# Kernel optimization log

Measured on AMD Instinct MI355X. Metric: run time of the kernel, lower is better.

Reference implementation:

```python
import jax, jax.numpy as jnp
import numpy as np

N, E, B = 20000, 320000, 64
HID, DEPTH, NFREQ = 128, 4, 8
NODE_DIM, EDGE_DIM, SG = 4, 3, 230
TWO_PI = 2.0 * np.pi


def setup_inputs() -> dict:
    key = jax.random.key(0)
    ks = jax.random.split(key, 20)
    inp = {}
    inp["x"] = jax.random.normal(ks[0], (N, NODE_DIM), jnp.float32)
    inp["edge_index"] = jax.random.randint(ks[1], (2, E), 0, N)
    inp["edge_attr"] = jax.random.normal(ks[2], (E, EDGE_DIM), jnp.float32)
    inp["batch"] = jnp.sort(jax.random.randint(ks[3], (N,), 0, B))
    inp["space_group"] = jax.random.randint(ks[4], (B,), 0, SG)
    inp["node_w"] = jax.random.normal(ks[5], (NODE_DIM, HID), jnp.float32) * 0.1
    inp["node_b"] = jnp.zeros((HID,), jnp.float32)
    inp["sg_table"] = jax.random.normal(ks[6], (SG, HID), jnp.float32) * 0.1
    inp["lin_w"] = jax.random.normal(ks[7], (DEPTH, 2 * HID + EDGE_DIM, HID), jnp.float32) * 0.05
    inp["lin_b"] = jnp.zeros((DEPTH, HID), jnp.float32)
    inp["att_w"] = jax.random.normal(ks[8], (DEPTH, 2 * HID + EDGE_DIM), jnp.float32) * 0.05
    inp["att_b"] = jnp.zeros((DEPTH,), jnp.float32)
    inp["fk_w"] = jax.random.normal(ks[9], (DEPTH, NFREQ, HID, HID), jnp.float32) * 0.1
    inp["fk_b"] = jnp.zeros((DEPTH, HID), jnp.float32)
    inp["bn_g"] = jnp.ones((DEPTH, HID), jnp.float32)
    inp["bn_b"] = jnp.zeros((DEPTH, HID), jnp.float32)
    inp["pool_w"] = jax.random.normal(ks[10], (HID,), jnp.float32) * 0.1
    inp["pool_b"] = jnp.zeros((), jnp.float32)
    inp["head_w1"] = jax.random.normal(ks[11], (4, 2 * HID, HID), jnp.float32) * 0.05
    inp["head_b1"] = jnp.zeros((4, HID), jnp.float32)
    for i, (nm, od) in enumerate([("e", 1), ("s", 3), ("c", 7), ("m", 3)]):
        inp[nm + "_w2"] = jax.random.normal(ks[12 + i], (HID, od), jnp.float32) * 0.05
        inp[nm + "_b2"] = jnp.zeros((od,), jnp.float32)
    return inp


def reference(x, edge_index, edge_attr, batch, space_group, node_w, node_b, sg_table,
              lin_w, lin_b, att_w, att_b, fk_w, fk_b, bn_g, bn_b, pool_w, pool_b,
              head_w1, head_b1, e_w2, e_b2, s_w2, s_b2, c_w2, c_b2, m_w2, m_b2):
    src, dst = edge_index[0], edge_index[1]  # x_j = x[src], x_i = x[dst]
    h = x @ node_w + node_b                  # [N, HID]
    sg = sg_table[space_group]               # [B, HID]
    freqs = jnp.arange(1, NFREQ + 1, dtype=h.dtype)
    for l in range(DEPTH):
        # edge conv: gather-concat-linear-sigmoid attention-scatter add
        tmp = jnp.concatenate([h[dst], h[src], edge_attr], axis=-1)   # [E, 2H+3]
        alpha = jax.nn.sigmoid(tmp @ att_w[l] + att_b[l])[:, None]    # [E, 1]
        msg = alpha * (tmp @ lin_w[l] + lin_b[l])                     # [E, H]
        h_conv = jax.ops.segment_sum(msg, dst, num_segments=N)
        # Fourier-Kolmogorov branch
        ang = TWO_PI * freqs[None, :, None] * h[:, None, :]           # [N, K, H]
        h_fk = (jnp.einsum('nki,kio->no', jnp.sin(ang), fk_w[l])
                + jnp.einsum('nki,kio->no', jnp.cos(ang), fk_w[l]) + fk_b[l])
        h = h_conv + h_fk
        # BatchNorm1d (batch statistics, training semantics) + ReLU; dropout = identity (eval)
        mu = h.mean(axis=0)
        var = h.var(axis=0)
        h = (h - mu) / jnp.sqrt(var + 1e-5) * bn_g[l] + bn_b[l]
        h = jax.nn.relu(h)
    # attention pool: softmax over ALL nodes (dim=0), as in the original
    a = jax.nn.softmax(h @ pool_w + pool_b, axis=0)[:, None]          # [N, 1]
    pooled = jax.ops.segment_sum(a * h, batch, num_segments=B)        # [B, H]
    comb = jnp.concatenate([pooled, sg], axis=-1)                     # [B, 2H]

    def head(i, w2, b2):
        z = jax.nn.relu(comb @ head_w1[i] + head_b1[i])
        return z @ w2 + b2

    energy = head(0, e_w2, e_b2)          # [B, 1]
    stability = head(1, s_w2, s_b2)       # [B, 3]
    crystal_system = head(2, c_w2, c_b2)  # [B, 7]
    material_type = head(3, m_w2, m_b2)   # [B, 3]
    return energy, stability, crystal_system, material_type
```

## Files before the change

### kernel.cpp

```cpp
#include <hip/hip_runtime.h>
#include <math.h>

#define HID 128
#define DEPTH 4
#define PSPLIT 16
#define SMAXB 40

typedef _Float16 half8 __attribute__((ext_vector_type(8)));
typedef float f4 __attribute__((ext_vector_type(4)));

__global__ void k_wsplit(const float* __restrict__ fkw, _Float16* __restrict__ whi,
                         _Float16* __restrict__ wlo) {
    __shared__ float sh[64][65];
    int bid = blockIdx.x;
    int l = bid >> 5; int r = bid & 31; int kb = r >> 1; int nbk = r & 1;
    const float* W = fkw + (size_t)l * 131072;
    _Float16* Hl = whi + (size_t)l * 131072;
    _Float16* Ll = wlo + (size_t)l * 131072;
    int k0 = kb * 64, n0 = nbk * 64;
    for (int i = threadIdx.x; i < 4096; i += 256) {
        int kk = i >> 6, nn = i & 63;
        sh[kk][nn] = W[(k0 + kk) * HID + n0 + nn];
    }
    __syncthreads();
    for (int i = threadIdx.x; i < 4096; i += 256) {
        int nn = i >> 6, kk = i & 63;
        float w = sh[kk][nn];
        _Float16 hi = (_Float16)w;
        _Float16 lo = (_Float16)((w - (float)hi) * 2048.f);
        Hl[(n0 + nn) * 1024 + k0 + kk] = hi;
        Ll[(n0 + nn) * 1024 + k0 + kk] = lo;
    }
}

__global__ void k_wsplit2(const float* __restrict__ linw, _Float16* __restrict__ lwhi,
                          _Float16* __restrict__ lwlo) {
    __shared__ float sh[64][65];
    int bid = blockIdx.x;
    int l = bid >> 3; int r = bid & 7; int cb = r >> 1; int kb = r & 1;
    const float* W = linw + (size_t)l * 259 * HID;
    int c0 = cb * 64, k0 = kb * 64;
    const float* base = W + (size_t)((c0 >= 128) ? 128 : 0) * HID + (c0 & 127);
    for (int i = threadIdx.x; i < 4096; i += 256) {
        int kk = i >> 6, cc = i & 63;
        sh[kk][cc] = base[(size_t)(k0 + kk) * HID + cc];
    }
    __syncthreads();
    _Float16* Hl = lwhi + (size_t)l * 32768;
    _Float16* Ll = lwlo + (size_t)l * 32768;
    for (int i = threadIdx.x; i < 4096; i += 256) {
        int cc = i >> 6, kk = i & 63;
        float w = sh[kk][cc];
        _Float16 hi = (_Float16)w;
        _Float16 lo = (_Float16)((w - (float)hi) * 2048.f);
        Hl[(size_t)(c0 + cc) * 128 + k0 + kk] = hi;
        Ll[(size_t)(c0 + cc) * 128 + k0 + kk] = lo;
    }
}

__global__ void k_hist(const int* __restrict__ dst, int* __restrict__ deg, int E) {
    int e = blockIdx.x * 256 + threadIdx.x;
    if (e < E) atomicAdd(&deg[dst[e]], 1);
}

__global__ void k_scan_a(const int* __restrict__ deg, int* __restrict__ bsum, int N) {
    __shared__ int sh[256];
    int i = blockIdx.x * 256 + threadIdx.x;
    sh[threadIdx.x] = (i < N) ? deg[i] : 0;
    __syncthreads();
    for (int off = 128; off > 0; off >>= 1) {
        if (threadIdx.x < (unsigned)off) sh[threadIdx.x] += sh[threadIdx.x + off];
        __syncthreads();
    }
    if (threadIdx.x == 0) bsum[blockIdx.x] = sh[0];
}

__global__ void k_scan_b(int* __restrict__ bsum, int nb) {
    __shared__ int sh[256];
    int v = (threadIdx.x < (unsigned)nb) ? bsum[threadIdx.x] : 0;
    sh[threadIdx.x] = v;
    __syncthreads();
    for (int off = 1; off < 256; off <<= 1) {
        int add = (threadIdx.x >= (unsigned)off) ? sh[threadIdx.x - off] : 0;
        __syncthreads();
        sh[threadIdx.x] += add;
        __syncthreads();
    }
    if (threadIdx.x < (unsigned)nb) bsum[threadIdx.x] = sh[threadIdx.x] - v;
}

__global__ void k_scan_c(const int* __restrict__ deg, const int* __restrict__ bsum,
                         int* __restrict__ offs, int* __restrict__ cursor, int N) {
    __shared__ int sh[256];
    int i = blockIdx.x * 256 + threadIdx.x;
    int v = (i < N) ? deg[i] : 0;
    sh[threadIdx.x] = v;
    __syncthreads();
    for (int off = 1; off < 256; off <<= 1) {
        int add = (threadIdx.x >= (unsigned)off) ? sh[threadIdx.x - off] : 0;
        __syncthreads();
        sh[threadIdx.x] += add;
        __syncthreads();
    }
    int ex = bsum[blockIdx.x] + sh[threadIdx.x] - v;
    if (i < N) { offs[i] = ex; cursor[i] = ex; }
    if (i == N - 1) offs[N] = ex + v;
}

__global__ void k_scatter(const int* __restrict__ src, const int* __restrict__ dst,
                          const float* __restrict__ ea, int* cursor,
                          int* __restrict__ srco, float4* __restrict__ ea3o, int E) {
    int e = blockIdx.x * 256 + threadIdx.x;
    if (e < E) {
        int d = dst[e];
        int p = atomicAdd(&cursor[d], 1);
        srco[p] = src[e];
        float4 q;
        q.x = ea[e * 3 + 0]; q.y = ea[e * 3 + 1]; q.z = ea[e * 3 + 2]; q.w = 0.f;
        ea3o[p] = q;
    }
}

__global__ void k_bstart(const int* __restrict__ batch, int* __restrict__ boffs, int N, int B) {
    int n = blockIdx.x * 256 + threadIdx.x;
    if (n >= N) return;
    int b1 = batch[n];
    if (n == 0) for (int b = 0; b <= b1; ++b) boffs[b] = 0;
    int b2 = (n + 1 < N) ? batch[n + 1] : B;
    for (int b = b1 + 1; b <= b2; ++b) boffs[b] = n + 1;
}

#define FK_MT 64
__global__ __launch_bounds__(512, 4) void k_gemms(const float* __restrict__ hsrc,
        const float* __restrict__ x, const float* __restrict__ nw, const float* __restrict__ nbv,
        const double* __restrict__ bnst, const float* __restrict__ bng, const float* __restrict__ bnb,
        int mode,
        const _Float16* __restrict__ whi, const _Float16* __restrict__ wlo,
        float* __restrict__ q0, float* __restrict__ q1,
        float* __restrict__ p2, float* __restrict__ p3,
        const _Float16* __restrict__ lwhi, const _Float16* __restrict__ lwlo,
        const float* __restrict__ linb,
        const float* __restrict__ attw, const float* __restrict__ attb,
        float* __restrict__ A1, float* __restrict__ A2,
        float* __restrict__ a1, float* __restrict__ a2,
        int FKB, int N) {
    __shared__ _Float16 ahi[FK_MT * 256];
    __shared__ _Float16 alo[FK_MT * 256];
    __shared__ float s_sc[128], s_sh[128];
    int tid = threadIdx.x;
    if (mode == 1) {
        if (tid < 128) {
            double invN = 1.0 / (double)N;
            float mu = (float)(bnst[tid] * invN);
            float var = (float)(bnst[128 + tid] * invN) - mu * mu;
            float inv = 1.f / sqrtf(var + 1e-5f);
            float sc = bng[tid] * inv;
            s_sc[tid] = sc;
            s_sh[tid] = bnb[tid] - mu * sc;
        }
        __syncthreads();
    }
    if (blockIdx.x < (unsigned)FKB) {
        int bx = blockIdx.x;
        int nb = (bx >> 2) * FK_MT;
        int ks = bx & 3;
        int kbase = ks * 256;
        int fr0 = kbase >> 7;
        {
            int row = tid >> 3;
            int o8 = tid & 7;
            int gn = nb + row;
            int rc = (gn < N) ? gn : (N - 1);
            float hv[2][8];
            if (mode == 0) {
                float4 xr = *(const float4*)&x[(size_t)rc * 4];
#pragma unroll
                for (int s = 0; s < 2; ++s)
#pragma unroll
                    for (int j = 0; j < 8; ++j) {
                        int c = s * 64 + o8 * 8 + j;
                        hv[s][j] = nbv[c] + xr.x * nw[c] + xr.y * nw[HID + c]
                                  + xr.z * nw[2 * HID + c] + xr.w * nw[3 * HID + c];
                    }
            } else {
                const float* hp = hsrc + (size_t)rc * HID + o8 * 8;
                *(float4*)&hv[0][0] = *(const float4*)hp;
                *(float4*)&hv[0][4] = *(const float4*)(hp + 4);
                *(float4*)&hv[1][0] = *(const float4*)(hp + 64);
                *(float4*)&hv[1][4] = *(const float4*)(hp + 68);
#pragma unroll
                for (int s = 0; s < 2; ++s)
#pragma unroll
                    for (int j = 0; j < 8; ++j) {
                        int c = s * 64 + o8 * 8 + j;
                        hv[s][j] = fmaxf(hv[s][j] * s_sc[c] + s_sh[c], 0.f);
                    }
            }
            int rs = row & 7;
#pragma unroll
            for (int g = 0; g < 2; ++g) {
                float freqf = 6.2831853f * (float)(fr0 + g + 1);
#pragma unroll
                for (int s = 0; s < 2; ++s) {
                    half8 vh, vl;
#pragma unroll
                    for (int j = 0; j < 8; ++j) {
                        float ang = freqf * hv[s][j] + 0.78539816f;
                        float a = 1.41421356f * __sinf(ang);
                        _Float16 hi = (_Float16)a;
                        vh[j] = hi;
                        vl[j] = (_Float16)((a - (float)hi) * 2048.f);
                    }
                    int oct = (g * 16 + s * 8 + o8) ^ rs;
                    *(half8*)&ahi[row * 256 + oct * 8] = vh;
                    *(half8*)&alo[row * 256 + oct * 8] = vl;
                }
            }
        }
        __syncthreads();
        int lane = tid & 63, wv = tid >> 6;
        int quad = lane >> 4, l16 = lane & 15;
        int n0w = wv * 16;
        f4 acc0[4], accL[4];
#pragma unroll
        for (int mi = 0; mi < 4; ++mi) { acc0[mi] = (f4)(0.f); accL[mi] = (f4)(0.f); }
        const _Float16* bhp = whi + (size_t)(n0w + l16) * 1024 + kbase + quad * 8;
        const _Float16* blp = wlo + (size_t)(n0w + l16) * 1024 + kbase + quad * 8;
        int rs16 = (l16 & 7) << 3;
#pragma unroll 2
        for (int step = 0; step < 8; ++step) {
            int ka = (step * 32 + quad * 8) ^ rs16;
            int ko = step * 32;
            half8 bh = *(const half8*)(bhp + ko);
            half8 bl = *(const half8*)(blp + ko);
            half8 ah[4], al[4];
#pragma unroll
            for (int mi = 0; mi < 4; ++mi) {
                ah[mi] = *(const half8*)&ahi[(l16 + mi * 16) * 256 + ka];
                al[mi] = *(const half8*)&alo[(l16 + mi * 16) * 256 + ka];
            }
#pragma unroll
            for (int mi = 0; mi < 4; ++mi) {
                acc0[mi] = __builtin_amdgcn_mfma_f32_16x16x32_f16(ah[mi], bh, acc0[mi], 0, 0, 0);
                accL[mi] = __builtin_amdgcn_mfma_f32_16x16x32_f16(ah[mi], bl, accL[mi], 0, 0, 0);
                accL[mi] = __builtin_amdgcn_mfma_f32_16x16x32_f16(al[mi], bh, accL[mi], 0, 0, 0);
            }
        }
        float* p = (ks == 0) ? q0 : (ks == 1) ? q1 : (ks == 2) ? p2 : p3;
        const float inv = 1.0f / 2048.0f;
#pragma unroll
        for (int mi = 0; mi < 4; ++mi)
#pragma unroll
            for (int r = 0; r < 4; ++r) {
                int gn = nb + mi * 16 + quad * 4 + r;
                if (gn < N)
                    p[gn * HID + n0w + l16] = acc0[mi][r] + accL[mi][r] * inv;
            }
    } else {
        int nb = (blockIdx.x - FKB) * 32;
        {
            int row = tid >> 4;
            int o16 = tid & 15;
            int gn = nb + row;
            int rc = (gn < N) ? gn : (N - 1);
            float hv[8];
            if (mode == 0) {
                float4 xr = *(const float4*)&x[(size_t)rc * 4];
#pragma unroll
                for (int j = 0; j < 8; ++j) {
                    int c = o16 * 8 + j;
                    hv[j] = nbv[c] + xr.x * nw[c] + xr.y * nw[HID + c]
                           + xr.z * nw[2 * HID + c] + xr.w * nw[3 * HID + c];
                }
            } else {
                const float* hp = hsrc + (size_t)rc * HID + o16 * 8;
                *(float4*)&hv[0] = *(const float4*)hp;
                *(float4*)&hv[4] = *(const float4*)(hp + 4);
#pragma unroll
                for (int j = 0; j < 8; ++j) {
                    int c = o16 * 8 + j;
                    hv[j] = fmaxf(hv[j] * s_sc[c] + s_sh[c], 0.f);
                }
            }
            float p1 = 0.f, p2d = 0.f;
#pragma unroll
            for (int j = 0; j < 8; ++j) {
                int k = o16 * 8 + j;
                p1 += hv[j] * attw[k];
                p2d += hv[j] * attw[128 + k];
            }
            for (int off = 8; off > 0; off >>= 1) {
                p1 += __shfl_down(p1, off, 16);
                p2d += __shfl_down(p2d, off, 16);
            }
            if (o16 == 0 && gn < N) {
                a1[gn] = p1 + attb[0];
                a2[gn] = p2d;
            }
            int rs = row & 7;
            half8 vh, vl;
#pragma unroll
            for (int j = 0; j < 8; ++j) {
                float a = hv[j];
                _Float16 hi = (_Float16)a;
                vh[j] = hi;
                vl[j] = (_Float16)((a - (float)hi) * 2048.f);
            }
            int oct = o16 ^ rs;
            *(half8*)&ahi[row * 128 + oct * 8] = vh;
            *(half8*)&alo[row * 128 + oct * 8] = vl;
        }
        __syncthreads();
        int lane = tid & 63, wv = tid >> 6;
        int quad = lane >> 4, l16 = lane & 15;
        int n0 = wv * 32;
        f4 acc0[2][2], accL[2][2];
#pragma unroll
        for (int mi = 0; mi < 2; ++mi)
#pragma unroll
            for (int ni = 0; ni < 2; ++ni) { acc0[mi][ni] = (f4)(0.f); accL[mi][ni] = (f4)(0.f); }
        const _Float16* bhp0 = lwhi + (size_t)(n0 + l16) * 128 + quad * 8;
        const _Float16* bhp1 = lwhi + (size_t)(n0 + 16 + l16) * 128 + quad * 8;
        const _Float16* blp0 = lwlo + (size_t)(n0 + l16) * 128 + quad * 8;
        const _Float16* blp1 = lwlo + (size_t)(n0 + 16 + l16) * 128 + quad * 8;
        int rs16 = (l16 & 7) << 3;
#pragma unroll
        for (int step = 0; step < 4; ++step) {
            int ka = (step * 32 + quad * 8) ^ rs16;
            int ko = step * 32;
            half8 bh0 = *(const half8*)(bhp0 + ko);
            half8 bh1 = *(const half8*)(bhp1 + ko);
            half8 bl0 = *(const half8*)(blp0 + ko);
            half8 bl1 = *(const half8*)(blp1 + ko);
            half8 ah[2], al[2];
#pragma unroll
            for (int mi = 0; mi < 2; ++mi) {
                ah[mi] = *(const half8*)&ahi[(l16 + mi * 16) * 128 + ka];
                al[mi] = *(const half8*)&alo[(l16 + mi * 16) * 128 + ka];
            }
#pragma unroll
            for (int mi = 0; mi < 2; ++mi) {
                acc0[mi][0] = __builtin_amdgcn_mfma_f32_16x16x32_f16(ah[mi], bh0, acc0[mi][0], 0, 0, 0);
                acc0[mi][1] = __builtin_amdgcn_mfma_f32_16x16x32_f16(ah[mi], bh1, acc0[mi][1], 0, 0, 0);
                accL[mi][0] = __builtin_amdgcn_mfma_f32_16x16x32_f16(ah[mi], bl0, accL[mi][0], 0, 0, 0);
                accL[mi][1] = __builtin_amdgcn_mfma_f32_16x16x32_f16(ah[mi], bl1, accL[mi][1], 0, 0, 0);
                accL[mi][0] = __builtin_amdgcn_mfma_f32_16x16x32_f16(al[mi], bh0, accL[mi][0], 0, 0, 0);
                accL[mi][1] = __builtin_amdgcn_mfma_f32_16x16x32_f16(al[mi], bh1, accL[mi][1], 0, 0, 0);
            }
        }
        const float inv = 1.0f / 2048.0f;
#pragma unroll
        for (int mi = 0; mi < 2; ++mi)
#pragma unroll
            for (int ni = 0; ni < 2; ++ni)
#pragma unroll
                for (int r = 0; r < 4; ++r) {
                    int gn = nb + mi * 16 + quad * 4 + r;
                    if (gn >= N) continue;
                    int cp = n0 + ni * 16 + l16;
                    float val = acc0[mi][ni][r] + accL[mi][ni][r] * inv;
                    if (cp < 128) A1[(size_t)gn * HID + cp] = val + linb[cp];
                    else          A2[(size_t)gn * HID + cp - 128] = val;
                }
    }
}

__global__ __launch_bounds__(256) void k_edge(const float* __restrict__ A1,
        const float* __restrict__ A2, const float* __restrict__ a1,
        const float* __restrict__ a2, const int* __restrict__ srco,
        const float4* __restrict__ ea3o, const int* __restrict__ offs,
        const float* __restrict__ linw3, const float* __restrict__ attw3,
        float* __restrict__ hconv, int N) {
    __shared__ float part[8][HID + 4];
    int n = blockIdx.x;
    int tid = threadIdx.x;
    int lane32 = tid & 31, slot = tid >> 5;
    int c4 = lane32 * 4;
    float4 w0v = *(const float4*)&linw3[c4];
    float4 w1v = *(const float4*)&linw3[HID + c4];
    float4 w2v = *(const float4*)&linw3[2 * HID + c4];
    float aw0 = attw3[0], aw1 = attw3[1], aw2 = attw3[2];
    float a1n = a1[n];
    float4 A1v = *(const float4*)&A1[(size_t)n * HID + c4];
    float4 acc; acc.x = acc.y = acc.z = acc.w = 0.f;
    int s0 = offs[n], s1 = offs[n + 1];
    for (int idx = s0 + slot; idx < s1; idx += 8) {
        int s = srco[idx];
        float4 q = ea3o[idx];
        float logit = a1n + a2[s] + q.x * aw0 + q.y * aw1 + q.z * aw2;
        float al = 1.f / (1.f + __expf(-logit));
        float4 a2v = *(const float4*)&A2[(size_t)s * HID + c4];
        float4 pre;
        pre.x = A1v.x + a2v.x + q.x * w0v.x + q.y * w1v.x + q.z * w2v.x;
        pre.y = A1v.y + a2v.y + q.x * w0v.y + q.y * w1v.y + q.z * w2v.y;
        pre.z = A1v.z + a2v.z + q.x * w0v.z + q.y * w1v.z + q.z * w2v.z;
        pre.w = A1v.w + a2v.w + q.x * w0v.w + q.y * w1v.w + q.z * w2v.w;
        acc.x += al * pre.x; acc.y += al * pre.y;
        acc.z += al * pre.z; acc.w += al * pre.w;
    }
    *(float4*)&part[slot][c4] = acc;
    __syncthreads();
    if (slot == 0) {
        float4 p = *(const float4*)&part[0][c4];
#pragma unroll
        for (int s = 1; s < 8; ++s) {
            float4 r = *(const float4*)&part[s][c4];
            p.x += r.x; p.y += r.y; p.z += r.z; p.w += r.w;
        }
        *(float4*)&hconv[(size_t)n * HID + c4] = p;
    }
}

__global__ __launch_bounds__(256) void k_bn_stats(float* __restrict__ hconv,
                           const float* __restrict__ p0, const float* __restrict__ p1,
                           const float* __restrict__ p2, const float* __restrict__ p3,
                           const float* __restrict__ fkb,
                           double* __restrict__ stats, int N) {
    int tid = threadIdx.x;
    int cq = tid & 31, rg = tid >> 5;
    int c4 = cq * 4;
    float4 bias = *(const float4*)&fkb[c4];
    float s1[4] = {0, 0, 0, 0}, s2[4] = {0, 0, 0, 0};
    for (int n = blockIdx.x * 8 + rg; n < N; n += gridDim.x * 8) {
        size_t idx = (size_t)n * HID + c4;
        float4 a  = *(const float4*)&hconv[idx];
        float4 b0 = *(const float4*)&p0[idx];
        float4 b1 = *(const float4*)&p1[idx];
        float4 b2 = *(const float4*)&p2[idx];
        float4 b3 = *(const float4*)&p3[idx];
        float4 v;
        v.x = a.x + b0.x + b1.x + b2.x + b3.x + bias.x;
        v.y = a.y + b0.y + b1.y + b2.y + b3.y + bias.y;
        v.z = a.z + b0.z + b1.z + b2.z + b3.z + bias.z;
        v.w = a.w + b0.w + b1.w + b2.w + b3.w + bias.w;
        *(float4*)&hconv[idx] = v;
        s1[0] += v.x; s2[0] += v.x * v.x;
        s1[1] += v.y; s2[1] += v.y * v.y;
        s1[2] += v.z; s2[2] += v.z * v.z;
        s1[3] += v.w; s2[3] += v.w * v.w;
    }
#pragma unroll
    for (int j = 0; j < 4; ++j) {
        s1[j] += __shfl_down(s1[j], 32);
        s2[j] += __shfl_down(s2[j], 32);
    }
    __shared__ float sh1[4][32][4], sh2[4][32][4];
    int wv = tid >> 6, lane = tid & 63;
    if (lane < 32) {
#pragma unroll
        for (int j = 0; j < 4; ++j) { sh1[wv][lane][j] = s1[j]; sh2[wv][lane][j] = s2[j]; }
    }
    __syncthreads();
    if (tid < 128) {
        int cq2 = tid >> 2, j2 = tid & 3;
        float t1 = sh1[0][cq2][j2] + sh1[1][cq2][j2] + sh1[2][cq2][j2] + sh1[3][cq2][j2];
        float t2 = sh2[0][cq2][j2] + sh2[1][cq2][j2] + sh2[2][cq2][j2] + sh2[3][cq2][j2];
        int c = cq2 * 4 + j2;
        atomicAdd(&stats[c], (double)t1);
        atomicAdd(&stats[128 + c], (double)t2);
    }
}

__global__ void k_bn_apply(const float* __restrict__ hsum, const double* __restrict__ stats,
                           const float* __restrict__ g, const float* __restrict__ b,
                           const float* __restrict__ pw, const float* __restrict__ pb,
                           float* __restrict__ h, float* __restrict__ s,
                           int do_score, int N) {
    int idx = blockIdx.x * 256 + threadIdx.x;
    int row = idx >> 5, cq = idx & 31;
    int c4 = cq * 4;
    int valid = row < N;
    double invN = 1.0 / (double)N;
    float p = 0.f;
    if (valid) {
        float4 hv = *(const float4*)&hsum[(size_t)row * HID + c4];
        float vin[4] = {hv.x, hv.y, hv.z, hv.w};
        float4 ov;
        float* po = &ov.x;
#pragma unroll
        for (int j = 0; j < 4; ++j) {
            int c = c4 + j;
            float mu = (float)(stats[c] * invN);
            float var = (float)(stats[128 + c] * invN) - mu * mu;
            float inv = 1.f / sqrtf(var + 1e-5f);
            float sc = g[c] * inv;
            float sh = b[c] - mu * sc;
            float oo = fmaxf(vin[j] * sc + sh, 0.f);
            po[j] = oo;
            if (do_score) p += oo * pw[c];
        }
        *(float4*)&h[(size_t)row * HID + c4] = ov;
    }
    if (do_score) {
        for (int off = 16; off > 0; off >>= 1) p += __shfl_down(p, off, 32);
        if ((threadIdx.x & 31) == 0 && valid) s[row] = p + pb[0];
    }
}

__global__ void k_smax1(const float* __restrict__ s, float* __restrict__ mzp, int N) {
    __shared__ float red[256];
    float m = -INFINITY;
    for (int n = blockIdx.x * 256 + threadIdx.x; n < N; n += SMAXB * 256)
        m = fmaxf(m, s[n]);
    red[threadIdx.x] = m;
    __syncthreads();
    for (int off = 128; off > 0; off >>= 1) {
        if (threadIdx.x < (unsigned)off)
            red[threadIdx.x] = fmaxf(red[threadIdx.x], red[threadIdx.x + off]);
        __syncthreads();
    }
    m = red[0];
    __syncthreads();
    float z = 0.f;
    for (int n = blockIdx.x * 256 + threadIdx.x; n < N; n += SMAXB * 256)
        z += __expf(s[n] - m);
    red[threadIdx.x] = z;
    __syncthreads();
    for (int off = 128; off > 0; off >>= 1) {
        if (threadIdx.x < (unsigned)off) red[threadIdx.x] += red[threadIdx.x + off];
        __syncthreads();
    }
    if (threadIdx.x == 0) { mzp[blockIdx.x * 2] = m; mzp[blockIdx.x * 2 + 1] = red[0]; }
}

__device__ __forceinline__ void combine_mz(const float* mzp, float& m, float& Z) {
    m = -INFINITY;
#pragma unroll 8
    for (int i = 0; i < SMAXB; ++i) m = fmaxf(m, mzp[i * 2]);
    Z = 0.f;
#pragma unroll 8
    for (int i = 0; i < SMAXB; ++i) Z += mzp[i * 2 + 1] * __expf(mzp[i * 2] - m);
}

__global__ void k_pool_part(const float* __restrict__ h, const float* __restrict__ s,
                            const float* __restrict__ mzp, const int* __restrict__ boffs,
                            float* __restrict__ part) {
    int b = blockIdx.x >> 4, split = blockIdx.x & (PSPLIT - 1);
    int c = threadIdx.x & 127, half = threadIdx.x >> 7;
    float m, Z;
    combine_mz(mzp, m, Z);
    (void)Z;
    int n0 = boffs[b], n1 = boffs[b + 1];
    float acc = 0.f;
    for (int n = n0 + split * 2 + half; n < n1; n += PSPLIT * 2)
        acc += __expf(s[n] - m) * h[n * HID + c];
    __shared__ float prt[2][HID];
    prt[half][c] = acc;
    __syncthreads();
    if (half == 0) part[(size_t)(b * PSPLIT + split) * HID + c] = prt[0][c] + prt[1][c];
}

__global__ __launch_bounds__(256) void k_head(const float* __restrict__ part,
                       const float* __restrict__ mzp,
                       const float* __restrict__ sg_table,
                       const int* __restrict__ space_group,
                       const float* __restrict__ hw1, const float* __restrict__ hb1,
                       const float* __restrict__ ew2, const float* __restrict__ eb2,
                       const float* __restrict__ sw2, const float* __restrict__ sb2,
                       const float* __restrict__ cw2, const float* __restrict__ cb2,
                       const float* __restrict__ mw2, const float* __restrict__ mb2,
                       float* __restrict__ out, int B) {
    __shared__ float comb[256];
    __shared__ float zred[2][128];
    __shared__ float zsh[128];
    int b = blockIdx.x >> 2, i = blockIdx.x & 3;
    int t = threadIdx.x;
    if (t < 128) {
        float m, Z;
        combine_mz(mzp, m, Z);
        float acc = 0.f;
#pragma unroll
        for (int j = 0; j < PSPLIT; ++j) acc += part[(size_t)(b * PSPLIT + j) * HID + t];
        comb[t] = acc / Z;
    } else {
        comb[t] = sg_table[space_group[b] * HID + (t - 128)];
    }
    __syncthreads();
    int half = t >> 7, tt = t & 127;
    const float* W = hw1 + ((size_t)i * 256 + half * 128) * HID;
    const float* cb = &comb[half * 128];
    float z = 0.f;
#pragma unroll 8
    for (int k = 0; k < 128; ++k) z += cb[k] * W[k * HID + tt];
    zred[half][tt] = z;
    __syncthreads();
    if (t < 128) zsh[t] = fmaxf(zred[0][t] + zred[1][t] + hb1[i * HID + t], 0.f);
    __syncthreads();
    const int od[4] = {1, 3, 7, 3};
    const int base[4] = {0, 64, 256, 704};
    const float* w2 = (i == 0) ? ew2 : (i == 1) ? sw2 : (i == 2) ? cw2 : mw2;
    const float* b2 = (i == 0) ? eb2 : (i == 1) ? sb2 : (i == 2) ? cb2 : mb2;
    int odi = od[i];
    if (t < odi) {
        float o = b2[t];
        for (int c = 0; c < HID; ++c) o += zsh[c] * w2[c * odi + t];
        out[base[i] + b * odi + t] = o;
    }
}

extern "C" void kernel_launch(void* const* d_in, const int* in_sizes, int n_in,
                              void* d_out, int out_size, void* d_ws, size_t ws_size,
                              hipStream_t stream) {
    const float* x          = (const float*)d_in[0];
    const int*   edge_index = (const int*)d_in[1];
    const float* edge_attr  = (const float*)d_in[2];
    const int*   batch      = (const int*)d_in[3];
    const int*   space_group= (const int*)d_in[4];
    const float* node_w     = (const float*)d_in[5];
    const float* node_b     = (const float*)d_in[6];
    const float* sg_table   = (const float*)d_in[7];
    const float* lin_w      = (const float*)d_in[8];
    const float* lin_b      = (const float*)d_in[9];
    const float* att_w      = (const float*)d_in[10];
    const float* att_b      = (const float*)d_in[11];
    const float* fk_w       = (const float*)d_in[12];
    const float* fk_b       = (const float*)d_in[13];
    const float* bn_g       = (const float*)d_in[14];
    const float* bn_b       = (const float*)d_in[15];
    const float* pool_w     = (const float*)d_in[16];
    const float* pool_b     = (const float*)d_in[17];
    const float* head_w1    = (const float*)d_in[18];
    const float* head_b1    = (const float*)d_in[19];
    const float* ew2 = (const float*)d_in[20]; const float* eb2 = (const float*)d_in[21];
    const float* sw2 = (const float*)d_in[22]; const float* sb2 = (const float*)d_in[23];
    const float* cw2 = (const float*)d_in[24]; const float* cb2 = (const float*)d_in[25];
    const float* mw2 = (const float*)d_in[26]; const float* mb2 = (const float*)d_in[27];
    float* out = (float*)d_out;

    const int N = in_sizes[3];
    const int E = in_sizes[1] / 2;
    const int B = in_sizes[4];
    const int* src = edge_index;
    const int* dst = edge_index + E;

    char* w = (char*)d_ws;
    auto alloc = [&](size_t bytes) { char* p = w; w += (bytes + 255) & ~(size_t)255; return p; };
    float*  h      = (float*)alloc((size_t)N * HID * 4);
    float*  A1     = (float*)alloc((size_t)N * HID * 4);
    float*  A2     = (float*)alloc((size_t)N * HID * 4);
    float*  q0     = (float*)alloc((size_t)N * HID * 4);
    float*  q1     = (float*)alloc((size_t)N * HID * 4);
    float*  p2     = (float*)alloc((size_t)N * HID * 4);
    float*  p3     = (float*)alloc((size_t)N * HID * 4);
    float*  hcv0   = (float*)alloc((size_t)N * HID * 4);
    float*  hcv1   = (float*)alloc((size_t)N * HID * 4);
    float*  a1     = (float*)alloc((size_t)N * 4);
    float*  a2     = (float*)alloc((size_t)N * 4);
    float*  sbuf   = (float*)alloc((size_t)N * 4);
    int*    deg    = (int*)alloc((size_t)N * 4);
    int*    cursor = (int*)alloc((size_t)N * 4);
    int*    offs   = (int*)alloc((size_t)(N + 1) * 4);
    int*    srco   = (int*)alloc((size_t)E * 4);
    float4* ea3o   = (float4*)alloc((size_t)E * 16);
    _Float16* whi  = (_Float16*)alloc((size_t)DEPTH * 1024 * HID * 2);
    _Float16* wlo  = (_Float16*)alloc((size_t)DEPTH * 1024 * HID * 2);
    _Float16* lwhi = (_Float16*)alloc((size_t)DEPTH * 256 * HID * 2);
    _Float16* lwlo = (_Float16*)alloc((size_t)DEPTH * 256 * HID * 2);
    int*    bsum   = (int*)alloc(256 * 4);
    int*    boffs  = (int*)alloc((size_t)(B + 1) * 4);
    double* stats  = (double*)alloc((size_t)DEPTH * 256 * 8);
    float*  mzp    = (float*)alloc(SMAXB * 2 * 4);
    float*  part   = (float*)alloc((size_t)B * PSPLIT * HID * 4);

    const int nchunk = (N + 255) / 256;
    const int echunk = (E + 255) / 256;
    const int FKB = ((N + FK_MT - 1) / FK_MT) * 4;
    const int NLB = (N + 31) / 32;

    k_wsplit<<<128, 256, 0, stream>>>(fk_w, whi, wlo);
    k_wsplit2<<<32, 256, 0, stream>>>(lin_w, lwhi, lwlo);
    hipMemsetAsync(deg, 0, (size_t)N * 4, stream);
    hipMemsetAsync(stats, 0, (size_t)DEPTH * 256 * 8, stream);
    k_hist<<<echunk, 256, 0, stream>>>(dst, deg, E);
    k_scan_a<<<nchunk, 256, 0, stream>>>(deg, bsum, N);
    k_scan_b<<<1, 256, 0, stream>>>(bsum, nchunk);
    k_scan_c<<<nchunk, 256, 0, stream>>>(deg, bsum, offs, cursor, N);
    k_scatter<<<echunk, 256, 0, stream>>>(src, dst, edge_attr, cursor, srco, ea3o, E);
    k_bstart<<<nchunk, 256, 0, stream>>>(batch, boffs, N, B);

    float* hcv[2] = {hcv0, hcv1};
    for (int l = 0; l < DEPTH; ++l) {
        const float* linw_l = lin_w + (size_t)l * 259 * HID;
        int mode = (l == 0) ? 0 : 1;
        const double* bst = (l == 0) ? (const double*)nullptr : stats + (size_t)(l - 1) * 256;
        const float* bgl = bn_g + (size_t)((l == 0) ? 0 : (l - 1)) * HID;
        const float* bbl = bn_b + (size_t)((l == 0) ? 0 : (l - 1)) * HID;
        const float* hprev = (l == 0) ? h : hcv[(l - 1) & 1];
        float* hcur = hcv[l & 1];
        k_gemms<<<FKB + NLB, 512, 0, stream>>>(
            hprev, x, node_w, node_b, bst, bgl, bbl, mode,
            whi + (size_t)l * 131072, wlo + (size_t)l * 131072, q0, q1, p2, p3,
            lwhi + (size_t)l * 32768, lwlo + (size_t)l * 32768,
            lin_b + l * HID, att_w + (size_t)l * 259, att_b + l,
            A1, A2, a1, a2, FKB, N);
        k_edge<<<N, 256, 0, stream>>>(A1, A2, a1, a2, srco, ea3o, offs,
                                      linw_l + 256 * HID, att_w + (size_t)l * 259 + 256,
                                      hcur, N);
        k_bn_stats<<<320, 256, 0, stream>>>(hcur, q0, q1, p2, p3, fk_b + l * HID,
                                            stats + (size_t)l * 256, N);
    }
    k_bn_apply<<<(N * 32 + 255) / 256, 256, 0, stream>>>(
        hcv[(DEPTH - 1) & 1], stats + (size_t)(DEPTH - 1) * 256,
        bn_g + (size_t)(DEPTH - 1) * HID, bn_b + (size_t)(DEPTH - 1) * HID,
        pool_w, pool_b, h, sbuf, 1, N);

    k_smax1<<<SMAXB, 256, 0, stream>>>(sbuf, mzp, N);
    k_pool_part<<<B * PSPLIT, 256, 0, stream>>>(h, sbuf, mzp, boffs, part);
    k_head<<<B * 4, 256, 0, stream>>>(part, mzp, sg_table, space_group, head_w1, head_b1,
                                      ew2, eb2, sw2, sb2, cw2, cb2, mw2, mb2, out, B);
}
```

Measured before the change: 625.7 us.

## Fuse partial-sum addition into edge kernel and pack four nodes per block

The edge aggregation kernel now processes four destination nodes per block, using two 32-lane slots per node instead of eight. This cuts the per-node block count and shrinks the shared-memory reduction. It also adds the four Fourier-kernel partial outputs and bias before writing, so the BN stats kernel only reads the final sum and no longer does a read-modify-write. The trade-off is less edge-level parallelism per node (two slots), which could hurt for high-degree nodes, and it saves roughly five tensor passes of global traffic per layer.

After: 624.1 us. About the same (-0.3%).

```diff
diff --git a/kernel.cpp b/kernel.cpp
--- a/kernel.cpp
+++ b/kernel.cpp
@@ -370,21 +370,31 @@
         const float* __restrict__ a2, const int* __restrict__ srco,
         const float4* __restrict__ ea3o, const int* __restrict__ offs,
         const float* __restrict__ linw3, const float* __restrict__ attw3,
-        float* __restrict__ hconv, int N) {
-    __shared__ float part[8][HID + 4];
-    int n = blockIdx.x;
+        const float* __restrict__ q0, const float* __restrict__ q1,
+        const float* __restrict__ p2s, const float* __restrict__ p3s,
+        const float* __restrict__ fkb,
+        float* __restrict__ hsum, int N) {
+    __shared__ float part[4][HID + 4];
     int tid = threadIdx.x;
-    int lane32 = tid & 31, slot = tid >> 5;
+    int nl = tid >> 6;
+    int slot = (tid >> 5) & 1;
+    int lane32 = tid & 31;
+    int n = blockIdx.x * 4 + nl;
     int c4 = lane32 * 4;
     float4 w0v = *(const float4*)&linw3[c4];
     float4 w1v = *(const float4*)&linw3[HID + c4];
     float4 w2v = *(const float4*)&linw3[2 * HID + c4];
     float aw0 = attw3[0], aw1 = attw3[1], aw2 = attw3[2];
-    float a1n = a1[n];
-    float4 A1v = *(const float4*)&A1[(size_t)n * HID + c4];
+    float a1n = 0.f;
+    float4 A1v; A1v.x = A1v.y = A1v.z = A1v.w = 0.f;
+    int s0 = 0, s1 = 0;
+    if (n < N) {
+        a1n = a1[n];
+        A1v = *(const float4*)&A1[(size_t)n * HID + c4];
+        s0 = offs[n]; s1 = offs[n + 1];
+    }
     float4 acc; acc.x = acc.y = acc.z = acc.w = 0.f;
-    int s0 = offs[n], s1 = offs[n + 1];
-    for (int idx = s0 + slot; idx < s1; idx += 8) {
+    for (int idx = s0 + slot; idx < s1; idx += 2) {
         int s = srco[idx];
         float4 q = ea3o[idx];
         float logit = a1n + a2[s] + q.x * aw0 + q.y * aw1 + q.z * aw2;
@@ -398,42 +408,35 @@
         acc.x += al * pre.x; acc.y += al * pre.y;
         acc.z += al * pre.z; acc.w += al * pre.w;
     }
-    *(float4*)&part[slot][c4] = acc;
-    __syncthreads();
-    if (slot == 0) {
-        float4 p = *(const float4*)&part[0][c4];
-#pragma unroll
-        for (int s = 1; s < 8; ++s) {
-            float4 r = *(const float4*)&part[s][c4];
-            p.x += r.x; p.y += r.y; p.z += r.z; p.w += r.w;
-        }
-        *(float4*)&hconv[(size_t)n * HID + c4] = p;
-    }
-}
-
-__global__ __launch_bounds__(256) void k_bn_stats(float* __restrict__ hconv,
-                           const float* __restrict__ p0, const float* __restrict__ p1,
-                           const float* __restrict__ p2, const float* __restrict__ p3,
-                           const float* __restrict__ fkb,
+    if (slot == 1) *(float4*)&part[nl][c4] = acc;
+    __syncthreads();
+    if (slot == 0 && n < N) {
+        float4 r = *(const float4*)&part[nl][c4];
+        float4 p;
+        p.x = acc.x + r.x; p.y = acc.y + r.y;
+        p.z = acc.z + r.z; p.w = acc.w + r.w;
+        size_t idx = (size_t)n * HID + c4;
+        float4 b0 = *(const float4*)&q0[idx];
+        float4 b1 = *(const float4*)&q1[idx];
+        float4 b2 = *(const float4*)&p2s[idx];
+        float4 b3 = *(const float4*)&p3s[idx];
+        float4 bias = *(const float4*)&fkb[c4];
+        p.x = p.x + b0.x + b1.x + b2.x + b3.x + bias.x;
+        p.y = p.y + b0.y + b1.y + b2.y + b3.y + bias.y;
+        p.z = p.z + b0.z + b1.z + b2.z + b3.z + bias.z;
+        p.w = p.w + b0.w + b1.w + b2.w + b3.w + bias.w;
+        *(float4*)&hsum[idx] = p;
+    }
+}
+
+__global__ __launch_bounds__(256) void k_bn_stats(const float* __restrict__ hsum,
                            double* __restrict__ stats, int N) {
     int tid = threadIdx.x;
     int cq = tid & 31, rg = tid >> 5;
     int c4 = cq * 4;
-    float4 bias = *(const float4*)&fkb[c4];
     float s1[4] = {0, 0, 0, 0}, s2[4] = {0, 0, 0, 0};
     for (int n = blockIdx.x * 8 + rg; n < N; n += gridDim.x * 8) {
-        size_t idx = (size_t)n * HID + c4;
-        float4 a  = *(const float4*)&hconv[idx];
-        float4 b0 = *(const float4*)&p0[idx];
-        float4 b1 = *(const float4*)&p1[idx];
-        float4 b2 = *(const float4*)&p2[idx];
-        float4 b3 = *(const float4*)&p3[idx];
-        float4 v;
-        v.x = a.x + b0.x + b1.x + b2.x + b3.x + bias.x;
-        v.y = a.y + b0.y + b1.y + b2.y + b3.y + bias.y;
-        v.z = a.z + b0.z + b1.z + b2.z + b3.z + bias.z;
-        v.w = a.w + b0.w + b1.w + b2.w + b3.w + bias.w;
-        *(float4*)&hconv[idx] = v;
+        float4 v = *(const float4*)&hsum[(size_t)n * HID + c4];
         s1[0] += v.x; s2[0] += v.x * v.x;
         s1[1] += v.y; s2[1] += v.y * v.y;
         s1[2] += v.z; s2[2] += v.z * v.z;
@@ -693,11 +696,11 @@
             lwhi + (size_t)l * 32768, lwlo + (size_t)l * 32768,
             lin_b + l * HID, att_w + (size_t)l * 259, att_b + l,
             A1, A2, a1, a2, FKB, N);
-        k_edge<<<N, 256, 0, stream>>>(A1, A2, a1, a2, srco, ea3o, offs,
+        k_edge<<<(N + 3) / 4, 256, 0, stream>>>(A1, A2, a1, a2, srco, ea3o, offs,
                                       linw_l + 256 * HID, att_w + (size_t)l * 259 + 256,
+                                      q0, q1, p2, p3, fk_b + l * HID,
                                       hcur, N);
-        k_bn_stats<<<320, 256, 0, stream>>>(hcur, q0, q1, p2, p3, fk_b + l * HID,
-                                            stats + (size_t)l * 256, N);
+        k_bn_stats<<<320, 256, 0, stream>>>(hcur, stats + (size_t)l * 256, N);
     }
     k_bn_apply<<<(N * 32 + 255) / 256, 256, 0, stream>>>(
         hcv[(DEPTH - 1) & 1], stats + (size_t)(DEPTH - 1) * 256,
```

## Co-schedule Fourier GEMM with edge aggregation in one launch, split linear GEMM out

Applied to the files above, without the earlier changes.

The small linear/attention GEMM now runs in its own kernel first. The Fourier-kernel GEMM blocks and the edge-aggregation blocks then share a single launch, so the memory-bound gather can overlap the MFMA-heavy FK GEMM. Edge blocks now handle 4 nodes per 512-thread block with 4 slots each, reusing the GEMM's shared memory for the partial-sum reduction. The cost is one extra launch, fewer slots per node on high-degree nodes, and the 64 KB LDS footprint now also applies to the edge blocks, which may limit their occupancy.

Result: slower. 685.9 us (+9.6%).

```diff
diff --git a/kernel.cpp b/kernel.cpp
--- a/kernel.cpp
+++ b/kernel.cpp
@@ -130,24 +130,20 @@
     for (int b = b1 + 1; b <= b2; ++b) boffs[b] = n + 1;
 }
 
-#define FK_MT 64
-__global__ __launch_bounds__(512, 4) void k_gemms(const float* __restrict__ hsrc,
+__global__ __launch_bounds__(512, 4) void k_nlgemm(const float* __restrict__ hsrc,
         const float* __restrict__ x, const float* __restrict__ nw, const float* __restrict__ nbv,
         const double* __restrict__ bnst, const float* __restrict__ bng, const float* __restrict__ bnb,
         int mode,
-        const _Float16* __restrict__ whi, const _Float16* __restrict__ wlo,
-        float* __restrict__ q0, float* __restrict__ q1,
-        float* __restrict__ p2, float* __restrict__ p3,
         const _Float16* __restrict__ lwhi, const _Float16* __restrict__ lwlo,
         const float* __restrict__ linb,
         const float* __restrict__ attw, const float* __restrict__ attb,
         float* __restrict__ A1, float* __restrict__ A2,
-        float* __restrict__ a1, float* __restrict__ a2,
-        int FKB, int N) {
-    __shared__ _Float16 ahi[FK_MT * 256];
-    __shared__ _Float16 alo[FK_MT * 256];
+        float* __restrict__ a1, float* __restrict__ a2, int N) {
+    __shared__ _Float16 ahi[32 * 128];
+    __shared__ _Float16 alo[32 * 128];
     __shared__ float s_sc[128], s_sh[128];
     int tid = threadIdx.x;
+    int nb = blockIdx.x * 32;
     if (mode == 1) {
         if (tid < 128) {
             double invN = 1.0 / (double)N;
@@ -160,7 +156,144 @@
         }
         __syncthreads();
     }
+    {
+        int row = tid >> 4;
+        int o16 = tid & 15;
+        int gn = nb + row;
+        int rc = (gn < N) ? gn : (N - 1);
+        float hv[8];
+        if (mode == 0) {
+            float4 xr = *(const float4*)&x[(size_t)rc * 4];
+#pragma unroll
+            for (int j = 0; j < 8; ++j) {
+                int c = o16 * 8 + j;
+                hv[j] = nbv[c] + xr.x * nw[c] + xr.y * nw[HID + c]
+                       + xr.z * nw[2 * HID + c] + xr.w * nw[3 * HID + c];
+            }
+        } else {
+            const float* hp = hsrc + (size_t)rc * HID + o16 * 8;
+            *(float4*)&hv[0] = *(const float4*)hp;
+            *(float4*)&hv[4] = *(const float4*)(hp + 4);
+#pragma unroll
+            for (int j = 0; j < 8; ++j) {
+                int c = o16 * 8 + j;
+                hv[j] = fmaxf(hv[j] * s_sc[c] + s_sh[c], 0.f);
+            }
+        }
+        float p1 = 0.f, p2 = 0.f;
+#pragma unroll
+        for (int j = 0; j < 8; ++j) {
+            int k = o16 * 8 + j;
+            p1 += hv[j] * attw[k];
+            p2 += hv[j] * attw[128 + k];
+        }
+        for (int off = 8; off > 0; off >>= 1) {
+            p1 += __shfl_down(p1, off, 16);
+            p2 += __shfl_down(p2, off, 16);
+        }
+        if (o16 == 0 && gn < N) {
+            a1[gn] = p1 + attb[0];
+            a2[gn] = p2;
+        }
+        int rs = row & 7;
+        half8 vh, vl;
+#pragma unroll
+        for (int j = 0; j < 8; ++j) {
+            float a = hv[j];
+            _Float16 hi = (_Float16)a;
+            vh[j] = hi;
+            vl[j] = (_Float16)((a - (float)hi) * 2048.f);
+        }
+        int oct = o16 ^ rs;
+        *(half8*)&ahi[row * 128 + oct * 8] = vh;
+        *(half8*)&alo[row * 128 + oct * 8] = vl;
+    }
+    __syncthreads();
+    int lane = tid & 63, wv = tid >> 6;
+    int quad = lane >> 4, l16 = lane & 15;
+    int n0 = wv * 32;
+    f4 acc0[2][2], accL[2][2];
+#pragma unroll
+    for (int mi = 0; mi < 2; ++mi)
+#pragma unroll
+        for (int ni = 0; ni < 2; ++ni) { acc0[mi][ni] = (f4)(0.f); accL[mi][ni] = (f4)(0.f); }
+    const _Float16* bhp0 = lwhi + (size_t)(n0 + l16) * 128 + quad * 8;
+    const _Float16* bhp1 = lwhi + (size_t)(n0 + 16 + l16) * 128 + quad * 8;
+    const _Float16* blp0 = lwlo + (size_t)(n0 + l16) * 128 + quad * 8;
+    const _Float16* blp1 = lwlo + (size_t)(n0 + 16 + l16) * 128 + quad * 8;
+    int rs16 = (l16 & 7) << 3;
+#pragma unroll
+    for (int step = 0; step < 4; ++step) {
+        int ka = (step * 32 + quad * 8) ^ rs16;
+        int ko = step * 32;
+        half8 bh0 = *(const half8*)(bhp0 + ko);
+        half8 bh1 = *(const half8*)(bhp1 + ko);
+        half8 bl0 = *(const half8*)(blp0 + ko);
+        half8 bl1 = *(const half8*)(blp1 + ko);
+        half8 ah[2], al[2];
+#pragma unroll
+        for (int mi = 0; mi < 2; ++mi) {
+            ah[mi] = *(const half8*)&ahi[(l16 + mi * 16) * 128 + ka];
+            al[mi] = *(const half8*)&alo[(l16 + mi * 16) * 128 + ka];
+        }
+#pragma unroll
+        for (int mi = 0; mi < 2; ++mi) {
+            acc0[mi][0] = __builtin_amdgcn_mfma_f32_16x16x32_f16(ah[mi], bh0, acc0[mi][0], 0, 0, 0);
+            acc0[mi][1] = __builtin_amdgcn_mfma_f32_16x16x32_f16(ah[mi], bh1, acc0[mi][1], 0, 0, 0);
+            accL[mi][0] = __builtin_amdgcn_mfma_f32_16x16x32_f16(ah[mi], bl0, accL[mi][0], 0, 0, 0);
+            accL[mi][1] = __builtin_amdgcn_mfma_f32_16x16x32_f16(ah[mi], bl1, accL[mi][1], 0, 0, 0);
+            accL[mi][0] = __builtin_amdgcn_mfma_f32_16x16x32_f16(al[mi], bh0, accL[mi][0], 0, 0, 0);
+            accL[mi][1] = __builtin_amdgcn_mfma_f32_16x16x32_f16(al[mi], bh1, accL[mi][1], 0, 0, 0);
+        }
+    }
+    const float inv = 1.0f / 2048.0f;
+#pragma unroll
+    for (int mi = 0; mi < 2; ++mi)
+#pragma unroll
+        for (int ni = 0; ni < 2; ++ni)
+#pragma unroll
+            for (int r = 0; r < 4; ++r) {
+                int gn = nb + mi * 16 + quad * 4 + r;
+                if (gn >= N) continue;
+                int cp = n0 + ni * 16 + l16;
+                float val = acc0[mi][ni][r] + accL[mi][ni][r] * inv;
+                if (cp < 128) A1[(size_t)gn * HID + cp] = val + linb[cp];
+                else          A2[(size_t)gn * HID + cp - 128] = val;
+            }
+}
+
+#define FK_MT 64
+__global__ __launch_bounds__(512, 4) void k_fkedge(const float* __restrict__ hsrc,
+        const float* __restrict__ x, const float* __restrict__ nw, const float* __restrict__ nbv,
+        const double* __restrict__ bnst, const float* __restrict__ bng, const float* __restrict__ bnb,
+        int mode,
+        const _Float16* __restrict__ whi, const _Float16* __restrict__ wlo,
+        float* __restrict__ q0, float* __restrict__ q1,
+        float* __restrict__ p2, float* __restrict__ p3,
+        const float* __restrict__ A1, const float* __restrict__ A2,
+        const float* __restrict__ a1, const float* __restrict__ a2,
+        const int* __restrict__ srco, const float4* __restrict__ ea3o,
+        const int* __restrict__ offs,
+        const float* __restrict__ linw3, const float* __restrict__ attw3,
+        float* __restrict__ hconv,
+        int FKB, int N) {
+    __shared__ _Float16 ahi[FK_MT * 256];
+    __shared__ _Float16 alo[FK_MT * 256];
+    __shared__ float s_sc[128], s_sh[128];
+    int tid = threadIdx.x;
     if (blockIdx.x < (unsigned)FKB) {
+        if (mode == 1) {
+            if (tid < 128) {
+                double invN = 1.0 / (double)N;
+                float mu = (float)(bnst[tid] * invN);
+                float var = (float)(bnst[128 + tid] * invN) - mu * mu;
+                float inv = 1.f / sqrtf(var + 1e-5f);
+                float sc = bng[tid] * inv;
+                s_sc[tid] = sc;
+                s_sh[tid] = bnb[tid] - mu * sc;
+            }
+            __syncthreads();
+        }
         int bx = blockIdx.x;
         int nb = (bx >> 2) * FK_MT;
         int ks = bx & 3;
@@ -257,157 +390,50 @@
                     p[gn * HID + n0w + l16] = acc0[mi][r] + accL[mi][r] * inv;
             }
     } else {
-        int nb = (blockIdx.x - FKB) * 32;
-        {
-            int row = tid >> 4;
-            int o16 = tid & 15;
-            int gn = nb + row;
-            int rc = (gn < N) ? gn : (N - 1);
-            float hv[8];
-            if (mode == 0) {
-                float4 xr = *(const float4*)&x[(size_t)rc * 4];
-#pragma unroll
-                for (int j = 0; j < 8; ++j) {
-                    int c = o16 * 8 + j;
-                    hv[j] = nbv[c] + xr.x * nw[c] + xr.y * nw[HID + c]
-                           + xr.z * nw[2 * HID + c] + xr.w * nw[3 * HID + c];
-                }
-            } else {
-                const float* hp = hsrc + (size_t)rc * HID + o16 * 8;
-                *(float4*)&hv[0] = *(const float4*)hp;
-                *(float4*)&hv[4] = *(const float4*)(hp + 4);
-#pragma unroll
-                for (int j = 0; j < 8; ++j) {
-                    int c = o16 * 8 + j;
-                    hv[j] = fmaxf(hv[j] * s_sc[c] + s_sh[c], 0.f);
-                }
-            }
-            float p1 = 0.f, p2d = 0.f;
-#pragma unroll
-            for (int j = 0; j < 8; ++j) {
-                int k = o16 * 8 + j;
-                p1 += hv[j] * attw[k];
-                p2d += hv[j] * attw[128 + k];
-            }
-            for (int off = 8; off > 0; off >>= 1) {
-                p1 += __shfl_down(p1, off, 16);
-                p2d += __shfl_down(p2d, off, 16);
-            }
-            if (o16 == 0 && gn < N) {
-                a1[gn] = p1 + attb[0];
-                a2[gn] = p2d;
-            }
-            int rs = row & 7;
-            half8 vh, vl;
-#pragma unroll
-            for (int j = 0; j < 8; ++j) {
-                float a = hv[j];
-                _Float16 hi = (_Float16)a;
-                vh[j] = hi;
-                vl[j] = (_Float16)((a - (float)hi) * 2048.f);
-            }
-            int oct = o16 ^ rs;
-            *(half8*)&ahi[row * 128 + oct * 8] = vh;
-            *(half8*)&alo[row * 128 + oct * 8] = vl;
-        }
-        __syncthreads();
-        int lane = tid & 63, wv = tid >> 6;
-        int quad = lane >> 4, l16 = lane & 15;
-        int n0 = wv * 32;
-        f4 acc0[2][2], accL[2][2];
-#pragma unroll
-        for (int mi = 0; mi < 2; ++mi)
-#pragma unroll
-            for (int ni = 0; ni < 2; ++ni) { acc0[mi][ni] = (f4)(0.f); accL[mi][ni] = (f4)(0.f); }
-        const _Float16* bhp0 = lwhi + (size_t)(n0 + l16) * 128 + quad * 8;
-        const _Float16* bhp1 = lwhi + (size_t)(n0 + 16 + l16) * 128 + quad * 8;
-        const _Float16* blp0 = lwlo + (size_t)(n0 + l16) * 128 + quad * 8;
-        const _Float16* blp1 = lwlo + (size_t)(n0 + 16 + l16) * 128 + quad * 8;
-        int rs16 = (l16 & 7) << 3;
-#pragma unroll
-        for (int step = 0; step < 4; ++step) {
-            int ka = (step * 32 + quad * 8) ^ rs16;
-            int ko = step * 32;
-            half8 bh0 = *(const half8*)(bhp0 + ko);
-            half8 bh1 = *(const half8*)(bhp1 + ko);
-            half8 bl0 = *(const half8*)(blp0 + ko);
-            half8 bl1 = *(const half8*)(blp1 + ko);
-            half8 ah[2], al[2];
-#pragma unroll
-            for (int mi = 0; mi < 2; ++mi) {
-                ah[mi] = *(const half8*)&ahi[(l16 + mi * 16) * 128 + ka];
-                al[mi] = *(const half8*)&alo[(l16 + mi * 16) * 128 + ka];
-            }
-#pragma unroll
-            for (int mi = 0; mi < 2; ++mi) {
-                acc0[mi][0] = __builtin_amdgcn_mfma_f32_16x16x32_f16(ah[mi], bh0, acc0[mi][0], 0, 0, 0);
-                acc0[mi][1] = __builtin_amdgcn_mfma_f32_16x16x32_f16(ah[mi], bh1, acc0[mi][1], 0, 0, 0);
-                accL[mi][0] = __builtin_amdgcn_mfma_f32_16x16x32_f16(ah[mi], bl0, accL[mi][0], 0, 0, 0);
-                accL[mi][1] = __builtin_amdgcn_mfma_f32_16x16x32_f16(ah[mi], bl1, accL[mi][1], 0, 0, 0);
-                accL[mi][0] = __builtin_amdgcn_mfma_f32_16x16x32_f16(al[mi], bh0, accL[mi][0], 0, 0, 0);
-                accL[mi][1] = __builtin_amdgcn_mfma_f32_16x16x32_f16(al[mi], bh1, accL[mi][1], 0, 0, 0);
-            }
-        }
-        const float inv = 1.0f / 2048.0f;
-#pragma unroll
-        for (int mi = 0; mi < 2; ++mi)
-#pragma unroll
-            for (int ni = 0; ni < 2; ++ni)
-#pragma unroll
-                for (int r = 0; r < 4; ++r) {
-                    int gn = nb + mi * 16 + quad * 4 + r;
-                    if (gn >= N) continue;
-                    int cp = n0 + ni * 16 + l16;
-                    float val = acc0[mi][ni][r] + accL[mi][ni][r] * inv;
-                    if (cp < 128) A1[(size_t)gn * HID + cp] = val + linb[cp];
-                    else          A2[(size_t)gn * HID + cp - 128] = val;
-                }
-    }
-}
-
-__global__ __launch_bounds__(256) void k_edge(const float* __restrict__ A1,
-        const float* __restrict__ A2, const float* __restrict__ a1,
-        const float* __restrict__ a2, const int* __restrict__ srco,
-        const float4* __restrict__ ea3o, const int* __restrict__ offs,
-        const float* __restrict__ linw3, const float* __restrict__ attw3,
-        float* __restrict__ hconv, int N) {
-    __shared__ float part[8][HID + 4];
-    int n = blockIdx.x;
-    int tid = threadIdx.x;
-    int lane32 = tid & 31, slot = tid >> 5;
-    int c4 = lane32 * 4;
-    float4 w0v = *(const float4*)&linw3[c4];
-    float4 w1v = *(const float4*)&linw3[HID + c4];
-    float4 w2v = *(const float4*)&linw3[2 * HID + c4];
-    float aw0 = attw3[0], aw1 = attw3[1], aw2 = attw3[2];
-    float a1n = a1[n];
-    float4 A1v = *(const float4*)&A1[(size_t)n * HID + c4];
-    float4 acc; acc.x = acc.y = acc.z = acc.w = 0.f;
-    int s0 = offs[n], s1 = offs[n + 1];
-    for (int idx = s0 + slot; idx < s1; idx += 8) {
-        int s = srco[idx];
-        float4 q = ea3o[idx];
-        float logit = a1n + a2[s] + q.x * aw0 + q.y * aw1 + q.z * aw2;
-        float al = 1.f / (1.f + __expf(-logit));
-        float4 a2v = *(const float4*)&A2[(size_t)s * HID + c4];
-        float4 pre;
-        pre.x = A1v.x + a2v.x + q.x * w0v.x + q.y * w1v.x + q.z * w2v.x;
-        pre.y = A1v.y + a2v.y + q.x * w0v.y + q.y * w1v.y + q.z * w2v.y;
-        pre.z = A1v.z + a2v.z + q.x * w0v.z + q.y * w1v.z + q.z * w2v.z;
-        pre.w = A1v.w + a2v.w + q.x * w0v.w + q.y * w1v.w + q.z * w2v.w;
-        acc.x += al * pre.x; acc.y += al * pre.y;
-        acc.z += al * pre.z; acc.w += al * pre.w;
-    }
-    *(float4*)&part[slot][c4] = acc;
-    __syncthreads();
-    if (slot == 0) {
-        float4 p = *(const float4*)&part[0][c4];
-#pragma unroll
-        for (int s = 1; s < 8; ++s) {
-            float4 r = *(const float4*)&part[s][c4];
-            p.x += r.x; p.y += r.y; p.z += r.z; p.w += r.w;
-        }
-        *(float4*)&hconv[(size_t)n * HID + c4] = p;
+        float* part = (float*)ahi;
+        int nl = tid >> 7;
+        int slot = (tid >> 5) & 3;
+        int lane32 = tid & 31;
+        int n = (blockIdx.x - FKB) * 4 + nl;
+        int c4 = lane32 * 4;
+        float4 w0v = *(const float4*)&linw3[c4];
+        float4 w1v = *(const float4*)&linw3[HID + c4];
+        float4 w2v = *(const float4*)&linw3[2 * HID + c4];
+        float aw0 = attw3[0], aw1 = attw3[1], aw2 = attw3[2];
+        float a1n = 0.f;
+        float4 A1v; A1v.x = A1v.y = A1v.z = A1v.w = 0.f;
+        int s0 = 0, s1 = 0;
+        if (n < N) {
+            a1n = a1[n];
+            A1v = *(const float4*)&A1[(size_t)n * HID + c4];
+            s0 = offs[n]; s1 = offs[n + 1];
+        }
+        float4 acc; acc.x = acc.y = acc.z = acc.w = 0.f;
+        for (int idx = s0 + slot; idx < s1; idx += 4) {
+            int s = srco[idx];
+            float4 q = ea3o[idx];
+            float logit = a1n + a2[s] + q.x * aw0 + q.y * aw1 + q.z * aw2;
+            float al = 1.f / (1.f + __expf(-logit));
+            float4 a2v = *(const float4*)&A2[(size_t)s * HID + c4];
+            float4 pre;
+            pre.x = A1v.x + a2v.x + q.x * w0v.x + q.y * w1v.x + q.z * w2v.x;
+            pre.y = A1v.y + a2v.y + q.x * w0v.y + q.y * w1v.y + q.z * w2v.y;
+            pre.z = A1v.z + a2v.z + q.x * w0v.z + q.y * w1v.z + q.z * w2v.z;
+            pre.w = A1v.w + a2v.w + q.x * w0v.w + q.y * w1v.w + q.z * w2v.w;
+            acc.x += al * pre.x; acc.y += al * pre.y;
+            acc.z += al * pre.z; acc.w += al * pre.w;
+        }
+        if (slot != 0)
+            *(float4*)&part[(nl * 3 + slot - 1) * (HID + 4) + c4] = acc;
+        __syncthreads();
+        if (slot == 0 && n < N) {
+#pragma unroll
+            for (int s = 0; s < 3; ++s) {
+                float4 r = *(const float4*)&part[(nl * 3 + s) * (HID + 4) + c4];
+                acc.x += r.x; acc.y += r.y; acc.z += r.z; acc.w += r.w;
+            }
+            *(float4*)&hconv[(size_t)n * HID + c4] = acc;
+        }
     }
 }
 
@@ -666,6 +692,7 @@
     const int echunk = (E + 255) / 256;
     const int FKB = ((N + FK_MT - 1) / FK_MT) * 4;
     const int NLB = (N + 31) / 32;
+    const int EB  = (N + 3) / 4;
 
     k_wsplit<<<128, 256, 0, stream>>>(fk_w, whi, wlo);
     k_wsplit2<<<32, 256, 0, stream>>>(lin_w, lwhi, lwlo);
@@ -687,15 +714,17 @@
         const float* bbl = bn_b + (size_t)((l == 0) ? 0 : (l - 1)) * HID;
         const float* hprev = (l == 0) ? h : hcv[(l - 1) & 1];
         float* hcur = hcv[l & 1];
-        k_gemms<<<FKB + NLB, 512, 0, stream>>>(
+        k_nlgemm<<<NLB, 512, 0, stream>>>(
+            hprev, x, node_w, node_b, bst, bgl, bbl, mode,
+            lwhi + (size_t)l * 32768, lwlo + (size_t)l * 32768,
+            lin_b + l * HID, att_w + (size_t)l * 259, att_b + l,
+            A1, A2, a1, a2, N);
+        k_fkedge<<<FKB + EB, 512, 0, stream>>>(
             hprev, x, node_w, node_b, bst, bgl, bbl, mode,
             whi + (size_t)l * 131072, wlo + (size_t)l * 131072, q0, q1, p2, p3,
-            lwhi + (size_t)l * 32768, lwlo + (size_t)l * 32768,
-            lin_b + l * HID, att_w + (size_t)l * 259, att_b + l,
-            A1, A2, a1, a2, FKB, N);
-        k_edge<<<N, 256, 0, stream>>>(A1, A2, a1, a2, srco, ea3o, offs,
-                                      linw_l + 256 * HID, att_w + (size_t)l * 259 + 256,
-                                      hcur, N);
+            A1, A2, a1, a2, srco, ea3o, offs,
+            linw_l + 256 * HID, att_w + (size_t)l * 259 + 256,
+            hcur, FKB, N);
         k_bn_stats<<<320, 256, 0, stream>>>(hcur, q0, q1, p2, p3, fk_b + l * HID,
                                             stats + (size_t)l * 256, N);
     }
```
